# Performance work log

Hardware: AMD Instinct MI355X
Metric: run time of the kernel (lower is better)

## Reference

```python
import jax, jax.numpy as jnp
import numpy as np

TAU = 10.0 / 7.0
V_TH = 1.0
ALPHA = 10.0  # sigmoid surrogate slope

@jax.custom_vjp
def spike_fn(v):
    # Heaviside(v - v_th) forward, sigmoid surrogate backward
    return (v >= V_TH).astype(v.dtype)

def _spike_fwd(v):
    return spike_fn(v), v

def _spike_bwd(v, g):
    s = jax.nn.sigmoid(ALPHA * (v - V_TH))
    return (g * ALPHA * s * (1.0 - s),)

spike_fn.defvjp(_spike_fwd, _spike_bwd)

def lif_multistep(x_bctm):
    # x: [B, C, T, M]; LIF recurrence over T axis, v_reset=0 hard reset,
    # decay_input=True: v = v + (x - v)/tau
    x_t = jnp.moveaxis(x_bctm, 2, 0)  # [T, B, C, M]
    def step(v, x):
        v = v + (x - v) / TAU
        s = spike_fn(v)
        v = v * (1.0 - s)  # hard reset to 0 (not detached)
        return v, s
    v0 = jnp.zeros_like(x_t[0])
    _, s_t = jax.lax.scan(step, v0, x_t)
    return jnp.moveaxis(s_t, 0, 2)  # [B, C, T, M]

def conv2d(x, w, pad, dil):
    return jax.lax.conv_general_dilated(
        x, w, window_strides=(1, 1),
        padding=[(pad[0], pad[0]), (pad[1], pad[1])],
        rhs_dilation=dil,
        dimension_numbers=('NCHW', 'OIHW', 'NCHW'))

def setup_inputs() -> dict:
    key = jax.random.key(0)
    k0, k1, k2, k3, k4 = jax.random.split(key, 5)
    B, T, M = 32, 128, 40
    x = jax.random.normal(k0, (B, 1, T, M), dtype=jnp.float32)
    # kaiming-ish init: std = 1/sqrt(fan_in)
    w1 = jax.random.normal(k1, (64, 1, 4, 3), dtype=jnp.float32) / np.sqrt(1 * 4 * 3)
    w2 = jax.random.normal(k2, (64, 64, 4, 3), dtype=jnp.float32) / np.sqrt(64 * 4 * 3)
    w3 = jax.random.normal(k3, (64, 64, 4, 3), dtype=jnp.float32) / np.sqrt(64 * 4 * 3)
    kw, kb = jax.random.split(k4)
    wf = jax.random.normal(kw, (12, 64 * 40), dtype=jnp.float32) / np.sqrt(64 * 40)
    bf = jnp.zeros((12,), dtype=jnp.float32)
    return {"x": x, "w1": w1, "w2": w2, "w3": w3, "wf": wf, "bf": bf}

def reference(x, w1, w2, w3, wf, bf):
    h = conv2d(x, w1, (2, 1), (1, 1))     # [B,64,T+1,40]
    h = lif_multistep(h)
    h = conv2d(h, w2, (6, 3), (4, 3))     # shape preserved
    h = lif_multistep(h)
    h = conv2d(h, w3, (24, 9), (16, 9))   # shape preserved
    h = lif_multistep(h)
    B, C, T, M = h.shape
    h = jnp.transpose(h, (0, 2, 1, 3)).reshape(B, T, C * M)  # flatten=True path
    y = h @ wf.T + bf                     # [B, T, 12]
    return y.mean(axis=1)                 # [B, 12]
```

## Files before the change

### kernel.cpp

```cpp
#include <hip/hip_runtime.h>


typedef __attribute__((ext_vector_type(8))) _Float16 v8h;
typedef __attribute__((ext_vector_type(16))) float v16f;
typedef _Float16 half_t;

#define NB 32
#define NC 64
#define NT 129
#define TIN 128
#define NM 40
#define MS8 80
#define ROWB8 3280
#define SROWB8 2560

__global__ void prep_wfrag(const float* __restrict__ w, uint4* __restrict__ wf) {
    int tid = blockIdx.x * 256 + threadIdx.x;
    if (tid >= 12288) return;
    int lane = tid & 63;
    int rest = tid >> 6;
    int hl = rest & 1;
    int ct = (rest >> 1) & 1;
    int cq = (rest >> 2) & 3;
    int tap = rest >> 4;
    int kh = tap / 3, kw = tap % 3;
    int co = ct * 32 + (lane & 31);
    unsigned short o[8];
#pragma unroll
    for (int jj = 0; jj < 8; jj++) {
        int ci = cq * 16 + (lane >> 5) * 8 + jj;
        float wv = w[((co * 64 + ci) * 4 + kh) * 3 + kw];
        _Float16 hi = (_Float16)wv;
        _Float16 val = hl ? (_Float16)((wv - (float)hi) * 2048.0f) : hi;
        unsigned short us;
        __builtin_memcpy(&us, &val, 2);
        o[jj] = us;
    }
    uint4 r;
    __builtin_memcpy(&r, o, 16);
    wf[tid] = r;
}

__global__ void conv1_lif1(const float* __restrict__ x, const float* __restrict__ w1,
                           unsigned char* __restrict__ s1) {
    const int mg = blockIdx.x;
    const int b = blockIdx.y;
    const int c = threadIdx.x & 63;
    const int ml = threadIdx.x >> 6;
    const int m = mg * 4 + ml;
    float w[4][3];
#pragma unroll
    for (int kh = 0; kh < 4; kh++)
#pragma unroll
        for (int kw = 0; kw < 3; kw++) w[kh][kw] = w1[(c * 4 + kh) * 3 + kw];
    const float* xb = x + (size_t)b * TIN * NM;

    float xw[12][3];
#pragma unroll
    for (int rr = 0; rr < 12; rr++)
#pragma unroll
        for (int kw = 0; kw < 3; kw++) xw[rr][kw] = 0.f;
#pragma unroll
    for (int rr = 2; rr < 4; rr++)
#pragma unroll
        for (int kw = 0; kw < 3; kw++) {
            int mc = m - 1 + kw;
            xw[rr][kw] = ((unsigned)mc < (unsigned)NM) ? xb[(rr - 2) * NM + mc] : 0.f;
        }

    unsigned char* orow = s1 + ((size_t)b * NT * NM + m) * 64 + c;
    float v = 0.f;
    const float TAUc = 10.0f / 7.0f;

    for (int tb = 0; tb < NT; tb += 8) {
#pragma unroll
        for (int q = 0; q < 8; q++) {
            int row = tb + 2 + q;
#pragma unroll
            for (int kw = 0; kw < 3; kw++) {
                int mc = m - 1 + kw;
                xw[4 + q][kw] = (row < TIN && (unsigned)mc < (unsigned)NM)
                                    ? xb[row * NM + mc] : 0.f;
            }
        }
        int kmax = (NT - tb) < 8 ? (NT - tb) : 8;
#pragma unroll
        for (int k = 0; k < 8; k++) {
            if (k < kmax) {
                float uacc = 0.f;
#pragma unroll
                for (int kh = 0; kh < 4; kh++)
#pragma unroll
                    for (int kw = 0; kw < 3; kw++) uacc += xw[k + kh][kw] * w[kh][kw];
                v = v + (uacc - v) / TAUc;
                orow[(size_t)(tb + k) * NM * 64] = (v >= 1.0f) ? 1 : 0;
                if (v >= 1.0f) v = 0.0f;
            }
        }
#pragma unroll
        for (int rr = 0; rr < 4; rr++)
#pragma unroll
            for (int kw = 0; kw < 3; kw++) xw[rr][kw] = xw[8 + rr][kw];
    }
}

__device__ inline v8h expand01(uint2 raw) {
    unsigned x0 = raw.x, x1 = raw.y;
    unsigned o0 = ((x0 & 0xFFu) | (((x0 >> 8) & 0xFFu) << 16)) * 0x3C00u;
    unsigned o1 = (((x0 >> 16) & 0xFFu) | ((x0 >> 24) << 16)) * 0x3C00u;
    unsigned o2 = ((x1 & 0xFFu) | (((x1 >> 8) & 0xFFu) << 16)) * 0x3C00u;
    unsigned o3 = (((x1 >> 16) & 0xFFu) | ((x1 >> 24) << 16)) * 0x3C00u;
    uint4 o = make_uint4(o0, o1, o2, o3);
    return __builtin_bit_cast(v8h, o);
}

template <int DH, int PH, int DW, int PW, int RMOD>
__global__ __launch_bounds__(256, 2) void convW(const unsigned char* __restrict__ spk,
                                                const uint4* __restrict__ wfrag,
                                                float* __restrict__ u) {
    __shared__ uint4 ldsq[11 * ROWB8 / 16];
    char* lds = (char*)ldsq;
    const int tid = threadIdx.x;
    const int lane = tid & 63;
    const int wp = tid >> 6;
    const int bx = blockIdx.x;
    const int b = blockIdx.y;
    int r, jj0;
    if (bx < 16) { r = bx % RMOD; jj0 = (bx / RMOD) * 8; }
    else         { r = 0;         jj0 = (16 / RMOD) * 8; }

    const char* spb = (const char*)spk + (size_t)b * NT * SROWB8;
#pragma unroll
    for (int k = 0; k < 8; k++) {
        int c = tid + k * 256;
        if (c < 1804) {
            int i = c / 164;
            int rem = c - i * 164;
            int s = rem >> 2;
            int q = rem & 3;
            int tg = r - PH + DH * (jj0 + i);
            uint4 val = make_uint4(0u, 0u, 0u, 0u);
            if ((unsigned)tg < (unsigned)NT && s < 40)
                val = *(const uint4*)(spb + ((size_t)tg * NM + s) * 64 + q * 16);
            *(uint4*)(lds + i * ROWB8 + s * MS8 + q * 16) = val;
        }
    }
    __syncthreads();

    const int pos = lane & 31;
    const int jl = pos >> 4;
    const int ml = pos & 15;
    const int hseg = lane >> 5;
    const int jj = jj0 + 2 * wp + jl;
    const int ldsrow = 2 * wp + jl;
    const int t = r + DH * jj;
    const int mtb[3] = {0, 16, 24};

    int P[3][3];
#pragma unroll
    for (int mt = 0; mt < 3; mt++)
#pragma unroll
        for (int kw = 0; kw < 3; kw++) {
            int md = mtb[mt] + ml + kw * DW - PW;
            int sel = ((unsigned)md < 40u) ? md : 40;
            P[mt][kw] = ldsrow * ROWB8 + sel * MS8 + hseg * 8;
        }

    v16f acc[3][2][2];
#pragma unroll
    for (int a = 0; a < 3; a++)
#pragma unroll
        for (int c2 = 0; c2 < 2; c2++)
#pragma unroll
            for (int h = 0; h < 2; h++) acc[a][c2][h] = (v16f)(0.0f);

#pragma unroll
    for (int tap = 0; tap < 12; tap++) {
        const int kh = tap / 3, kw = tap % 3;
#pragma unroll
        for (int cq = 0; cq < 4; cq++) {
            const uint4* wq = wfrag + (tap * 4 + cq) * 256 + lane;
            uint4 a00 = wq[0];
            uint4 a01 = wq[64];
            uint4 a10 = wq[128];
            uint4 a11 = wq[192];
            uint2 r0 = *(const uint2*)(lds + P[0][kw] + kh * ROWB8 + cq * 16);
            uint2 r1 = *(const uint2*)(lds + P[1][kw] + kh * ROWB8 + cq * 16);
            uint2 r2 = *(const uint2*)(lds + P[2][kw] + kh * ROWB8 + cq * 16);
            v8h B0 = expand01(r0);
            v8h B1 = expand01(r1);
            v8h B2 = expand01(r2);
            v8h A00 = __builtin_bit_cast(v8h, a00);
            v8h A01 = __builtin_bit_cast(v8h, a01);
            v8h A10 = __builtin_bit_cast(v8h, a10);
            v8h A11 = __builtin_bit_cast(v8h, a11);
            acc[0][0][0] = __builtin_amdgcn_mfma_f32_32x32x16_f16(A00, B0, acc[0][0][0], 0, 0, 0);
            acc[0][0][1] = __builtin_amdgcn_mfma_f32_32x32x16_f16(A01, B0, acc[0][0][1], 0, 0, 0);
            acc[0][1][0] = __builtin_amdgcn_mfma_f32_32x32x16_f16(A10, B0, acc[0][1][0], 0, 0, 0);
            acc[0][1][1] = __builtin_amdgcn_mfma_f32_32x32x16_f16(A11, B0, acc[0][1][1], 0, 0, 0);
            acc[1][0][0] = __builtin_amdgcn_mfma_f32_32x32x16_f16(A00, B1, acc[1][0][0], 0, 0, 0);
            acc[1][0][1] = __builtin_amdgcn_mfma_f32_32x32x16_f16(A01, B1, acc[1][0][1], 0, 0, 0);
            acc[1][1][0] = __builtin_amdgcn_mfma_f32_32x32x16_f16(A10, B1, acc[1][1][0], 0, 0, 0);
            acc[1][1][1] = __builtin_amdgcn_mfma_f32_32x32x16_f16(A11, B1, acc[1][1][1], 0, 0, 0);
            acc[2][0][0] = __builtin_amdgcn_mfma_f32_32x32x16_f16(A00, B2, acc[2][0][0], 0, 0, 0);
            acc[2][0][1] = __builtin_amdgcn_mfma_f32_32x32x16_f16(A01, B2, acc[2][0][1], 0, 0, 0);
            acc[2][1][0] = __builtin_amdgcn_mfma_f32_32x32x16_f16(A10, B2, acc[2][1][0], 0, 0, 0);
            acc[2][1][1] = __builtin_amdgcn_mfma_f32_32x32x16_f16(A11, B2, acc[2][1][1], 0, 0, 0);
        }
    }

    const float invs = 1.0f / 2048.0f;
    if (t < NT) {
#pragma unroll
        for (int mt = 0; mt < 3; mt++) {
            int m = mtb[mt] + ml;
            float* base = u + ((size_t)(b * NT + t) * NM + m) * 64;
#pragma unroll
            for (int ct = 0; ct < 2; ct++) {
#pragma unroll
                for (int g = 0; g < 4; g++) {
                    int co = ct * 32 + 8 * g + 4 * hseg;
                    float4 val;
                    val.x = acc[mt][ct][0][4 * g + 0] + acc[mt][ct][1][4 * g + 0] * invs;
                    val.y = acc[mt][ct][0][4 * g + 1] + acc[mt][ct][1][4 * g + 1] * invs;
                    val.z = acc[mt][ct][0][4 * g + 2] + acc[mt][ct][1][4 * g + 2] * invs;
                    val.w = acc[mt][ct][0][4 * g + 3] + acc[mt][ct][1][4 * g + 3] * invs;
                    *(float4*)(base + co) = val;
                }
            }
        }
    }
}

__global__ void lif_spikes(const float* __restrict__ u, unsigned char* __restrict__ s2) {
    int tid = blockIdx.x * 256 + threadIdx.x;
    int b = tid / 2560;
    int cm = tid % 2560;
    const float* up = u + (size_t)b * NT * 2560 + cm;
    unsigned char* sp = s2 + (size_t)b * NT * 2560 + cm;
    float v = 0.f;
    const float TAUc = 10.0f / 7.0f;
    for (int tb = 0; tb < 128; tb += 16) {
        float uu[16];
#pragma unroll
        for (int k = 0; k < 16; k++) uu[k] = up[(size_t)(tb + k) * 2560];
#pragma unroll
        for (int k = 0; k < 16; k++) {
            v = v + (uu[k] - v) / TAUc;
            sp[(size_t)(tb + k) * 2560] = (v >= 1.0f) ? 1 : 0;
            if (v >= 1.0f) v = 0.f;
        }
    }
    float uu = up[(size_t)128 * 2560];
    v = v + (uu - v) / TAUc;
    sp[(size_t)128 * 2560] = (v >= 1.0f) ? 1 : 0;
}

__global__ void lif_sum(const float* __restrict__ u, float* __restrict__ hsum) {
    int tid = blockIdx.x * 256 + threadIdx.x;
    int b = tid / 2560;
    int cm = tid % 2560;
    int m = cm >> 6;
    int co = cm & 63;
    const float* up = u + (size_t)b * NT * 2560 + cm;
    float v = 0.f, cnt = 0.f;
    const float TAUc = 10.0f / 7.0f;
    for (int tb = 0; tb < 128; tb += 16) {
        float uu[16];
#pragma unroll
        for (int k = 0; k < 16; k++) uu[k] = up[(size_t)(tb + k) * 2560];
#pragma unroll
        for (int k = 0; k < 16; k++) {
            v = v + (uu[k] - v) / TAUc;
            if (v >= 1.0f) { cnt += 1.0f; v = 0.f; }
        }
    }
    float uu = up[(size_t)128 * 2560];
    v = v + (uu - v) / TAUc;
    if (v >= 1.0f) cnt += 1.0f;
    hsum[b * 2560 + co * NM + m] = cnt;
}

__global__ void fc_out(const float* __restrict__ hsum, const float* __restrict__ wf,
                       const float* __restrict__ bfv, float* __restrict__ out) {
    int b = blockIdx.x;
    int tid = threadIdx.x;
    float p[12];
#pragma unroll
    for (int k = 0; k < 12; k++) p[k] = 0.0f;
    for (int cm = tid; cm < NC * NM; cm += 256) {
        float h = hsum[b * NC * NM + cm];
#pragma unroll
        for (int k = 0; k < 12; k++) p[k] += h * wf[k * (NC * NM) + cm];
    }
    __shared__ float red[12][4];
    int lane = tid & 63, w = tid >> 6;
#pragma unroll
    for (int k = 0; k < 12; k++) {
        float s = p[k];
#pragma unroll
        for (int off = 32; off > 0; off >>= 1) s += __shfl_down(s, off, 64);
        if (lane == 0) red[k][w] = s;
    }
    __syncthreads();
    if (tid < 12) {
        float s = red[tid][0] + red[tid][1] + red[tid][2] + red[tid][3];
        out[b * 12 + tid] = bfv[tid] + s / 129.0f;
    }
}

extern "C" void kernel_launch(void* const* d_in, const int* in_sizes, int n_in,
                              void* d_out, int out_size, void* d_ws, size_t ws_size,
                              hipStream_t stream) {
    const float* x  = (const float*)d_in[0];
    const float* w1 = (const float*)d_in[1];
    const float* w2 = (const float*)d_in[2];
    const float* w3 = (const float*)d_in[3];
    const float* wf = (const float*)d_in[4];
    const float* bf = (const float*)d_in[5];
    float* out = (float*)d_out;

    char* ws = (char*)d_ws;
    unsigned char* s1 = (unsigned char*)ws;
    unsigned char* s2 = (unsigned char*)(ws + 10567680);
    float*  u   = (float*)(ws + 21135360);
    uint4*  wf2 = (uint4*)(ws + 63406080);
    uint4*  wf3 = (uint4*)(ws + 63602688);
    float* hsum = (float*)(ws + 63799296);

    prep_wfrag<<<48, 256, 0, stream>>>(w2, wf2);
    prep_wfrag<<<48, 256, 0, stream>>>(w3, wf3);

    conv1_lif1<<<dim3(10, 32), 256, 0, stream>>>(x, w1, s1);

    convW<4, 6, 3, 3, 4><<<dim3(17, 32), 256, 0, stream>>>(s1, wf2, u);
    lif_spikes<<<320, 256, 0, stream>>>(u, s2);

    convW<16, 24, 9, 9, 16><<<dim3(17, 32), 256, 0, stream>>>(s2, wf3, u);
    lif_sum<<<320, 256, 0, stream>>>(u, hsum);

    fc_out<<<32, 256, 0, stream>>>(hsum, wf, bf, out);
}
```

Measured before the change: 243.8 us.

## Split fp16 hi/lo weight halves across waves and reduce through LDS

New measurement: 218.9 us. 1.11x faster.

```diff
diff --git a/kernel.cpp b/kernel.cpp
--- a/kernel.cpp
+++ b/kernel.cpp
@@ -105,35 +105,36 @@
 }
 
 __device__ inline v8h expand01(uint2 raw) {
-    unsigned x0 = raw.x, x1 = raw.y;
-    unsigned o0 = ((x0 & 0xFFu) | (((x0 >> 8) & 0xFFu) << 16)) * 0x3C00u;
-    unsigned o1 = (((x0 >> 16) & 0xFFu) | ((x0 >> 24) << 16)) * 0x3C00u;
-    unsigned o2 = ((x1 & 0xFFu) | (((x1 >> 8) & 0xFFu) << 16)) * 0x3C00u;
-    unsigned o3 = (((x1 >> 16) & 0xFFu) | ((x1 >> 24) << 16)) * 0x3C00u;
+    unsigned o0 = __builtin_amdgcn_perm(0u, raw.x, 0x04010400u) * 0x3C00u;
+    unsigned o1 = __builtin_amdgcn_perm(0u, raw.x, 0x04030402u) * 0x3C00u;
+    unsigned o2 = __builtin_amdgcn_perm(0u, raw.y, 0x04010400u) * 0x3C00u;
+    unsigned o3 = __builtin_amdgcn_perm(0u, raw.y, 0x04030402u) * 0x3C00u;
     uint4 o = make_uint4(o0, o1, o2, o3);
     return __builtin_bit_cast(v8h, o);
 }
 
 template <int DH, int PH, int DW, int PW, int RMOD>
-__global__ __launch_bounds__(256, 2) void convW(const unsigned char* __restrict__ spk,
+__global__ __launch_bounds__(256, 3) void convW(const unsigned char* __restrict__ spk,
                                                 const uint4* __restrict__ wfrag,
                                                 float* __restrict__ u) {
-    __shared__ uint4 ldsq[11 * ROWB8 / 16];
+    __shared__ uint4 ldsq[7 * ROWB8 / 16];
     char* lds = (char*)ldsq;
     const int tid = threadIdx.x;
     const int lane = tid & 63;
-    const int wp = tid >> 6;
+    const int wv = tid >> 6;
+    const int wp = wv >> 1;
+    const int hl = wv & 1;
     const int bx = blockIdx.x;
     const int b = blockIdx.y;
     int r, jj0;
-    if (bx < 16) { r = bx % RMOD; jj0 = (bx / RMOD) * 8; }
-    else         { r = 0;         jj0 = (16 / RMOD) * 8; }
+    if (bx < 32) { r = bx % RMOD; jj0 = (bx / RMOD) * 4; }
+    else         { r = 0;         jj0 = (32 / RMOD) * 4; }
 
     const char* spb = (const char*)spk + (size_t)b * NT * SROWB8;
 #pragma unroll
-    for (int k = 0; k < 8; k++) {
+    for (int k = 0; k < 5; k++) {
         int c = tid + k * 256;
-        if (c < 1804) {
+        if (c < 1148) {
             int i = c / 164;
             int rem = c - i * 164;
             int s = rem >> 2;
@@ -166,69 +167,75 @@
             P[mt][kw] = ldsrow * ROWB8 + sel * MS8 + hseg * 8;
         }
 
-    v16f acc[3][2][2];
+    v16f acc[3][2];
 #pragma unroll
     for (int a = 0; a < 3; a++)
 #pragma unroll
-        for (int c2 = 0; c2 < 2; c2++)
-#pragma unroll
-            for (int h = 0; h < 2; h++) acc[a][c2][h] = (v16f)(0.0f);
-
+        for (int c2 = 0; c2 < 2; c2++) acc[a][c2] = (v16f)(0.0f);
+
+    const int hl64 = hl * 64;
 #pragma unroll
     for (int tap = 0; tap < 12; tap++) {
         const int kh = tap / 3, kw = tap % 3;
 #pragma unroll
         for (int cq = 0; cq < 4; cq++) {
-            const uint4* wq = wfrag + (tap * 4 + cq) * 256 + lane;
-            uint4 a00 = wq[0];
-            uint4 a01 = wq[64];
-            uint4 a10 = wq[128];
-            uint4 a11 = wq[192];
+            const uint4* wq = wfrag + (tap * 4 + cq) * 256 + hl64 + lane;
+            uint4 a0 = wq[0];
+            uint4 a1 = wq[128];
             uint2 r0 = *(const uint2*)(lds + P[0][kw] + kh * ROWB8 + cq * 16);
             uint2 r1 = *(const uint2*)(lds + P[1][kw] + kh * ROWB8 + cq * 16);
             uint2 r2 = *(const uint2*)(lds + P[2][kw] + kh * ROWB8 + cq * 16);
             v8h B0 = expand01(r0);
             v8h B1 = expand01(r1);
             v8h B2 = expand01(r2);
-            v8h A00 = __builtin_bit_cast(v8h, a00);
-            v8h A01 = __builtin_bit_cast(v8h, a01);
-            v8h A10 = __builtin_bit_cast(v8h, a10);
-            v8h A11 = __builtin_bit_cast(v8h, a11);
-            acc[0][0][0] = __builtin_amdgcn_mfma_f32_32x32x16_f16(A00, B0, acc[0][0][0], 0, 0, 0);
-            acc[0][0][1] = __builtin_amdgcn_mfma_f32_32x32x16_f16(A01, B0, acc[0][0][1], 0, 0, 0);
-            acc[0][1][0] = __builtin_amdgcn_mfma_f32_32x32x16_f16(A10, B0, acc[0][1][0], 0, 0, 0);
-            acc[0][1][1] = __builtin_amdgcn_mfma_f32_32x32x16_f16(A11, B0, acc[0][1][1], 0, 0, 0);
-            acc[1][0][0] = __builtin_amdgcn_mfma_f32_32x32x16_f16(A00, B1, acc[1][0][0], 0, 0, 0);
-            acc[1][0][1] = __builtin_amdgcn_mfma_f32_32x32x16_f16(A01, B1, acc[1][0][1], 0, 0, 0);
-            acc[1][1][0] = __builtin_amdgcn_mfma_f32_32x32x16_f16(A10, B1, acc[1][1][0], 0, 0, 0);
-            acc[1][1][1] = __builtin_amdgcn_mfma_f32_32x32x16_f16(A11, B1, acc[1][1][1], 0, 0, 0);
-            acc[2][0][0] = __builtin_amdgcn_mfma_f32_32x32x16_f16(A00, B2, acc[2][0][0], 0, 0, 0);
-            acc[2][0][1] = __builtin_amdgcn_mfma_f32_32x32x16_f16(A01, B2, acc[2][0][1], 0, 0, 0);
-            acc[2][1][0] = __builtin_amdgcn_mfma_f32_32x32x16_f16(A10, B2, acc[2][1][0], 0, 0, 0);
-            acc[2][1][1] = __builtin_amdgcn_mfma_f32_32x32x16_f16(A11, B2, acc[2][1][1], 0, 0, 0);
+            v8h A0 = __builtin_bit_cast(v8h, a0);
+            v8h A1 = __builtin_bit_cast(v8h, a1);
+            acc[0][0] = __builtin_amdgcn_mfma_f32_32x32x16_f16(A0, B0, acc[0][0], 0, 0, 0);
+            acc[0][1] = __builtin_amdgcn_mfma_f32_32x32x16_f16(A1, B0, acc[0][1], 0, 0, 0);
+            acc[1][0] = __builtin_amdgcn_mfma_f32_32x32x16_f16(A0, B1, acc[1][0], 0, 0, 0);
+            acc[1][1] = __builtin_amdgcn_mfma_f32_32x32x16_f16(A1, B1, acc[1][1], 0, 0, 0);
+            acc[2][0] = __builtin_amdgcn_mfma_f32_32x32x16_f16(A0, B2, acc[2][0], 0, 0, 0);
+            acc[2][1] = __builtin_amdgcn_mfma_f32_32x32x16_f16(A1, B2, acc[2][1], 0, 0, 0);
         }
     }
 
     const float invs = 1.0f / 2048.0f;
-    if (t < NT) {
-#pragma unroll
-        for (int mt = 0; mt < 3; mt++) {
+    float4* lred = (float4*)lds;
+    __syncthreads();
+#pragma unroll
+    for (int mt = 0; mt < 3; mt++) {
+        if (hl) {
+#pragma unroll
+            for (int ct = 0; ct < 2; ct++)
+#pragma unroll
+                for (int g = 0; g < 4; g++) {
+                    float4 vv;
+                    vv.x = acc[mt][ct][4 * g + 0];
+                    vv.y = acc[mt][ct][4 * g + 1];
+                    vv.z = acc[mt][ct][4 * g + 2];
+                    vv.w = acc[mt][ct][4 * g + 3];
+                    lred[(wp * 8 + ct * 4 + g) * 64 + lane] = vv;
+                }
+        }
+        __syncthreads();
+        if (!hl && t < NT) {
             int m = mtb[mt] + ml;
             float* base = u + ((size_t)(b * NT + t) * NM + m) * 64;
 #pragma unroll
-            for (int ct = 0; ct < 2; ct++) {
+            for (int ct = 0; ct < 2; ct++)
 #pragma unroll
                 for (int g = 0; g < 4; g++) {
+                    float4 lo = lred[(wp * 8 + ct * 4 + g) * 64 + lane];
                     int co = ct * 32 + 8 * g + 4 * hseg;
                     float4 val;
-                    val.x = acc[mt][ct][0][4 * g + 0] + acc[mt][ct][1][4 * g + 0] * invs;
-                    val.y = acc[mt][ct][0][4 * g + 1] + acc[mt][ct][1][4 * g + 1] * invs;
-                    val.z = acc[mt][ct][0][4 * g + 2] + acc[mt][ct][1][4 * g + 2] * invs;
-                    val.w = acc[mt][ct][0][4 * g + 3] + acc[mt][ct][1][4 * g + 3] * invs;
+                    val.x = acc[mt][ct][4 * g + 0] + lo.x * invs;
+                    val.y = acc[mt][ct][4 * g + 1] + lo.y * invs;
+                    val.z = acc[mt][ct][4 * g + 2] + lo.z * invs;
+                    val.w = acc[mt][ct][4 * g + 3] + lo.w * invs;
                     *(float4*)(base + co) = val;
                 }
-            }
-        }
+        }
+        __syncthreads();
     }
 }
 
@@ -333,10 +340,10 @@
 
     conv1_lif1<<<dim3(10, 32), 256, 0, stream>>>(x, w1, s1);
 
-    convW<4, 6, 3, 3, 4><<<dim3(17, 32), 256, 0, stream>>>(s1, wf2, u);
+    convW<4, 6, 3, 3, 4><<<dim3(33, 32), 256, 0, stream>>>(s1, wf2, u);
     lif_spikes<<<320, 256, 0, stream>>>(u, s2);
 
-    convW<16, 24, 9, 9, 16><<<dim3(17, 32), 256, 0, stream>>>(s2, wf3, u);
+    convW<16, 24, 9, 9, 16><<<dim3(33, 32), 256, 0, stream>>>(s2, wf3, u);
     lif_sum<<<320, 256, 0, stream>>>(u, hsum);
 
     fc_out<<<32, 256, 0, stream>>>(hsum, wf, bf, out);
```
